# Optimization experiments

Measured on AMD Instinct MI355X. Metric: run time of the kernel, lower is better.

Reference implementation:

```python
import jax, jax.numpy as jnp
import numpy as np

N = 50000      # query points
N0 = 50000     # support points
M = 32         # neighbors per query
K = 15         # kernel points
DIM = 3
D_IN = 64
D_OUT = 64
POINT_INFLUENCE = 1.0
KERNEL_RADIUS = 1.5 * POINT_INFLUENCE  # _INFLUENCE_TO_RADIUS * point_influence


def setup_inputs() -> dict:
    key = jax.random.key(0)
    k1, k2, k3, k4, k5 = jax.random.split(key, 5)
    query_points = jax.random.normal(k1, (N, DIM), jnp.float32)
    support_points = jax.random.normal(k2, (N0, DIM), jnp.float32)
    neighbors = jax.random.randint(k3, (N, M), 0, N0 + 1)  # index N0 = shadow point
    x = jax.random.normal(k4, (N0, D_IN), jnp.float32)
    # Kernel point dispositions: fixed center point, rest spread within kernel radius
    # (stand-in for kernel_point_optimization_debug; K_points is a frozen parameter).
    rng = np.random.RandomState(0)
    kp = rng.uniform(-1.0, 1.0, (K, DIM))
    kp[0, :] = 0.0
    kp = kp * (KERNEL_RADIUS / np.max(np.linalg.norm(kp, axis=1)))
    K_points = jnp.asarray(kp, dtype=jnp.float32)
    # Xavier-normal conv weights [K, D_IN, D_OUT]
    std = (2.0 / (D_IN + D_OUT)) ** 0.5
    weight = jax.random.normal(k5, (K, D_IN, D_OUT), jnp.float32) * std
    return {
        "query_points": query_points,
        "support_points": support_points,
        "neighbors": neighbors,
        "x": x,
        "K_points": K_points,
        "weight": weight,
    }


def reference(query_points, support_points, neighbors, x, K_points, weight):
    # Shadow support point far away + zero shadow feature row
    shadow = jnp.full((1, query_points.shape[1]), 1e6, dtype=support_points.dtype)
    sp = jnp.concatenate([support_points, shadow], axis=0)            # [N0+1, 3]
    xp = jnp.concatenate([x, jnp.zeros((1, x.shape[1]), x.dtype)], axis=0)  # [N0+1, d]

    # Gather neighbor coords, center on query point
    neighb_pts = sp[neighbors] - query_points[:, None, :]             # [N, M, 3]
    # Squared distances to each kernel point
    diff = neighb_pts[:, :, None, :] - K_points[None, None, :, :]     # [N, M, K, 3]
    sq_distances = jnp.sum(diff * diff, axis=-1)                      # [N, M, K]

    # Linear influence, then transpose to [N, K, M]
    all_weights = jnp.clip(1.0 - jnp.sqrt(sq_distances) / POINT_INFLUENCE, 0.0)
    all_weights = jnp.swapaxes(all_weights, 1, 2)                     # [N, K, M]

    # Gather neighbor features and aggregate per kernel point
    feats = xp[neighbors]                                             # [N, M, d]
    weighted = jnp.einsum("nkm,nmd->nkd", all_weights, feats)        # [N, K, d]
    # Apply per-kernel-point weight matrices and sum over kernel points
    out = jnp.einsum("nkd,kdo->no", weighted, weight)                # [N, out]
    return out
```

## Files before the change

### kernel.cpp

```cpp
#include <hip/hip_runtime.h>

#define NQ 50000
#define NS 50000
#define MNB 32
#define KP 15
#define DF 64
#define WTS 968

typedef __bf16 bf16x8 __attribute__((ext_vector_type(8)));
typedef float  f32x4  __attribute__((ext_vector_type(4)));

__device__ __forceinline__ unsigned short f2bf(float f) {
    union { float f; unsigned int u; } v; v.f = f;
    unsigned int u = v.u;
    return (unsigned short)((u + 0x7FFFu + ((u >> 16) & 1u)) >> 16);
}

__global__ __launch_bounds__(256) void conv_w(const float* __restrict__ W,
                                              uint4* __restrict__ wBf) {
    const int chunk = blockIdx.x * 256 + threadIdx.x;
    if (chunk >= 7680) return;
    const int t = chunk >> 6, c = chunk & 63;
    union { unsigned short s[8]; uint4 u; } pk;
    #pragma unroll
    for (int j = 0; j < 8; ++j)
        pk.s[j] = f2bf(W[(size_t)(t * 8 + j) * 64 + c]);
    wBf[chunk] = pk.u;
}

__global__ __launch_bounds__(1024, 8) void kpconv_fused(
    const float* __restrict__ qp, const float* __restrict__ sp,
    const int* __restrict__ nb, const float* __restrict__ x,
    const float* __restrict__ kpts, const uint4* __restrict__ wBf,
    float* __restrict__ out)
{
    __shared__ struct {
        __align__(16) unsigned short wt[16 * WTS];
        __align__(16) float w[16][33][20];
        __align__(16) unsigned int am[16][MNB];
    } sm;

    const int tid  = threadIdx.x;
    const int lane = tid & 63, wv = tid >> 6;
    const int kh = lane >> 5, m = lane & 31;
    const int n0 = blockIdx.x * 16;
    const int n  = n0 + wv;

    if (lane < 20) sm.w[wv][32][lane] = 0.0f;

    const int id = nb[n * MNB + m];
    const float qx = qp[n * 3 + 0], qy = qp[n * 3 + 1], qz = qp[n * 3 + 2];
    float sx = 1e6f, sy = 1e6f, sz = 1e6f;
    if (id < NS) { sx = sp[id * 3 + 0]; sy = sp[id * 3 + 1]; sz = sp[id * 3 + 2]; }
    const float rx = sx - qx, ry = sy - qy, rz = sz - qz;
    float wk[8], wmax = 0.0f;
    const int kbase = kh * 8;
    #pragma unroll
    for (int j = 0; j < 8; ++j) {
        const int k = kbase + j;
        const int kc = (k < KP) ? k : 0;
        const float dx = rx - kpts[kc * 3 + 0];
        const float dy = ry - kpts[kc * 3 + 1];
        const float dz = rz - kpts[kc * 3 + 2];
        float wkj = fmaxf(1.0f - sqrtf(dx * dx + dy * dy + dz * dz), 0.0f);
        if (k >= KP) wkj = 0.0f;
        wk[j] = wkj;
        wmax = fmaxf(wmax, wkj);
    }
    const unsigned long long bal = __ballot(wmax > 0.0f);
    const unsigned int comb = (unsigned int)(bal & 0xFFFFFFFFull) |
                              (unsigned int)(bal >> 32);
    const int A = __popc(comb);
    const int Apad = (A + 3) & ~3;
    const bool act = (comb >> m) & 1u;
    if (act) {
        float4* wr = (float4*)&sm.w[wv][m][0];
        wr[kh * 2 + 0] = make_float4(wk[0], wk[1], wk[2], wk[3]);
        wr[kh * 2 + 1] = make_float4(wk[4], wk[5], wk[6], wk[7]);
    }
    if (kh == 0) {
        if (act) {
            const int pos = __popc(comb & ((1u << m) - 1u));
            sm.am[wv][pos] = ((unsigned)id << 6) | (unsigned)m;
        }
        if (m < Apad - A) sm.am[wv][A + m] = 32u;
    }

    const int d = lane;
    float acc[KP];
    #pragma unroll
    for (int k = 0; k < KP; ++k) acc[k] = 0.0f;

#define ACC1(EE, FF)                                                        \
    {                                                                       \
        const float4* wr = (const float4*)&sm.w[wv][(EE) & 63u][0];         \
        const float4 w0 = wr[0], w1 = wr[1], w2 = wr[2], w3 = wr[3];        \
        acc[0]  += (FF) * w0.x;  acc[1]  += (FF) * w0.y;                    \
        acc[2]  += (FF) * w0.z;  acc[3]  += (FF) * w0.w;                    \
        acc[4]  += (FF) * w1.x;  acc[5]  += (FF) * w1.y;                    \
        acc[6]  += (FF) * w1.z;  acc[7]  += (FF) * w1.w;                    \
        acc[8]  += (FF) * w2.x;  acc[9]  += (FF) * w2.y;                    \
        acc[10] += (FF) * w2.z;  acc[11] += (FF) * w2.w;                    \
        acc[12] += (FF) * w3.x;  acc[13] += (FF) * w3.y;  acc[14] += (FF) * w3.z; \
    }

    for (int j0 = 0; j0 < Apad; j0 += 4) {
        const uint4 e = *(const uint4*)&sm.am[wv][j0];
        const float f0 = x[(size_t)(e.x >> 6) * DF + d];
        const float f1 = x[(size_t)(e.y >> 6) * DF + d];
        const float f2 = x[(size_t)(e.z >> 6) * DF + d];
        const float f3 = x[(size_t)(e.w >> 6) * DF + d];
        ACC1(e.x, f0) ACC1(e.y, f1) ACC1(e.z, f2) ACC1(e.w, f3)
    }
#undef ACC1

    unsigned short* wrow = sm.wt + wv * WTS + d;
    #pragma unroll
    for (int k = 0; k < KP; ++k)
        wrow[k * DF] = f2bf(acc[k]);

    __syncthreads();
    if (wv >= 4) return;

    const int cl = lane & 15, q = lane >> 4;
    f32x4 dacc = (f32x4){0.f, 0.f, 0.f, 0.f};
    #pragma unroll 6
    for (int ks = 0; ks < 30; ++ks) {
        const bf16x8 a = *(const bf16x8*)&sm.wt[cl * WTS + ks * 32 + q * 8];
        union { uint4 u; bf16x8 v; } bu;
        bu.u = wBf[(4 * ks + q) * 64 + wv * 16 + cl];
        dacc = __builtin_amdgcn_mfma_f32_16x16x32_bf16(a, bu.v, dacc, 0, 0, 0);
    }
    #pragma unroll
    for (int i = 0; i < 4; ++i)
        out[(size_t)(n0 + q * 4 + i) * 64 + wv * 16 + cl] = dacc[i];
}

extern "C" void kernel_launch(void* const* d_in, const int* in_sizes, int n_in,
                              void* d_out, int out_size, void* d_ws, size_t ws_size,
                              hipStream_t stream) {
    const float* qp   = (const float*)d_in[0];
    const float* sp   = (const float*)d_in[1];
    const int*   nb   = (const int*)d_in[2];
    const float* x    = (const float*)d_in[3];
    const float* kpts = (const float*)d_in[4];
    const float* W    = (const float*)d_in[5];
    float* out = (float*)d_out;

    uint4* wBf = (uint4*)d_ws;

    hipLaunchKernelGGL(conv_w, dim3(30), dim3(256), 0, stream, W, wBf);
    hipLaunchKernelGGL(kpconv_fused, dim3(NQ / 16), dim3(1024), 0, stream,
                       qp, sp, nb, x, kpts, wBf, out);
}
```

Measured before the change: 140.6 us.

## Aggregate neighbor features with bf16 MFMA over pre-converted bf16 features

Replaces the per-lane scalar FMA loop that accumulated neighbor features into 15 kernel-point sums with a single 16x16x32 bf16 MFMA per 16-channel block. Neighbor weights are stored as bf16 in shared memory and neighbor features are gathered from a bf16 copy of x made by a new conversion kernel each call. The conv weight layout is permuted to match the new intermediate ordering. The ballot-based compaction that skipped inactive neighbors is dropped, so all 32 neighbors are always gathered. It also adds a full read and write pass over x and rounds features to bf16, which lowers precision.

```diff
diff --git a/kernel.cpp b/kernel.cpp
--- a/kernel.cpp
+++ b/kernel.cpp
@@ -6,6 +6,7 @@
 #define KP 15
 #define DF 64
 #define WTS 968
+#define WQS 40
 
 typedef __bf16 bf16x8 __attribute__((ext_vector_type(8)));
 typedef float  f32x4  __attribute__((ext_vector_type(4)));
@@ -16,28 +17,48 @@
     return (unsigned short)((u + 0x7FFFu + ((u >> 16) & 1u)) >> 16);
 }
 
+__global__ __launch_bounds__(256) void conv_x(const float* __restrict__ x,
+                                              unsigned int* __restrict__ xb, int n4) {
+    const int i = blockIdx.x * 256 + threadIdx.x;
+    if (i * 4 + 3 < n4) {
+        const float4* s = (const float4*)x + i * 2;
+        const float4 a0 = s[0], a1 = s[1];
+        uint4 o;
+        o.x = (unsigned)f2bf(a0.x) | ((unsigned)f2bf(a0.y) << 16);
+        o.y = (unsigned)f2bf(a0.z) | ((unsigned)f2bf(a0.w) << 16);
+        o.z = (unsigned)f2bf(a1.x) | ((unsigned)f2bf(a1.y) << 16);
+        o.w = (unsigned)f2bf(a1.z) | ((unsigned)f2bf(a1.w) << 16);
+        ((uint4*)xb)[i] = o;
+    }
+}
+
 __global__ __launch_bounds__(256) void conv_w(const float* __restrict__ W,
                                               uint4* __restrict__ wBf) {
     const int chunk = blockIdx.x * 256 + threadIdx.x;
     if (chunk >= 7680) return;
-    const int t = chunk >> 6, c = chunk & 63;
+    const int tc = chunk >> 6, c = chunk & 63;
     union { unsigned short s[8]; uint4 u; } pk;
     #pragma unroll
-    for (int j = 0; j < 8; ++j)
-        pk.s[j] = f2bf(W[(size_t)(t * 8 + j) * 64 + c]);
+    for (int j = 0; j < 8; ++j) {
+        const int kappa = tc * 8 + j;
+        const int k  = kappa >> 6;
+        const int cb = kappa & 3;
+        const int t  = (kappa >> 2) & 15;
+        pk.s[j] = f2bf(W[(size_t)(k * 64 + cb * 16 + t) * 64 + c]);
+    }
     wBf[chunk] = pk.u;
 }
 
 __global__ __launch_bounds__(1024, 8) void kpconv_fused(
     const float* __restrict__ qp, const float* __restrict__ sp,
-    const int* __restrict__ nb, const float* __restrict__ x,
+    const int* __restrict__ nb, const unsigned short* __restrict__ xbu,
     const float* __restrict__ kpts, const uint4* __restrict__ wBf,
     float* __restrict__ out)
 {
     __shared__ struct {
         __align__(16) unsigned short wt[16 * WTS];
-        __align__(16) float w[16][33][20];
-        __align__(16) unsigned int am[16][MNB];
+        __align__(16) unsigned short wq[16][16 * WQS];
+        __align__(16) unsigned int   ids[16][MNB];
     } sm;
 
     const int tid  = threadIdx.x;
@@ -46,83 +67,66 @@
     const int n0 = blockIdx.x * 16;
     const int n  = n0 + wv;
 
-    if (lane < 20) sm.w[wv][32][lane] = 0.0f;
-
     const int id = nb[n * MNB + m];
     const float qx = qp[n * 3 + 0], qy = qp[n * 3 + 1], qz = qp[n * 3 + 2];
     float sx = 1e6f, sy = 1e6f, sz = 1e6f;
     if (id < NS) { sx = sp[id * 3 + 0]; sy = sp[id * 3 + 1]; sz = sp[id * 3 + 2]; }
     const float rx = sx - qx, ry = sy - qy, rz = sz - qz;
-    float wk[8], wmax = 0.0f;
-    const int kbase = kh * 8;
+    float wk[8];
     #pragma unroll
     for (int j = 0; j < 8; ++j) {
-        const int k = kbase + j;
+        const int k = kh * 8 + j;
         const int kc = (k < KP) ? k : 0;
         const float dx = rx - kpts[kc * 3 + 0];
         const float dy = ry - kpts[kc * 3 + 1];
         const float dz = rz - kpts[kc * 3 + 2];
-        float wkj = fmaxf(1.0f - sqrtf(dx * dx + dy * dy + dz * dz), 0.0f);
-        if (k >= KP) wkj = 0.0f;
-        wk[j] = wkj;
-        wmax = fmaxf(wmax, wkj);
+        wk[j] = fmaxf(1.0f - sqrtf(dx * dx + dy * dy + dz * dz), 0.0f);
     }
-    const unsigned long long bal = __ballot(wmax > 0.0f);
-    const unsigned int comb = (unsigned int)(bal & 0xFFFFFFFFull) |
-                              (unsigned int)(bal >> 32);
-    const int A = __popc(comb);
-    const int Apad = (A + 3) & ~3;
-    const bool act = (comb >> m) & 1u;
-    if (act) {
-        float4* wr = (float4*)&sm.w[wv][m][0];
-        wr[kh * 2 + 0] = make_float4(wk[0], wk[1], wk[2], wk[3]);
-        wr[kh * 2 + 1] = make_float4(wk[4], wk[5], wk[6], wk[7]);
+    #pragma unroll
+    for (int j = 0; j < 8; ++j) {
+        const int k = kh * 8 + j;
+        if (k < KP) sm.wq[wv][k * WQS + m] = f2bf(wk[j]);
     }
-    if (kh == 0) {
-        if (act) {
-            const int pos = __popc(comb & ((1u << m) - 1u));
-            sm.am[wv][pos] = ((unsigned)id << 6) | (unsigned)m;
-        }
-        if (m < Apad - A) sm.am[wv][A + m] = 32u;
+    if (kh == 0) sm.ids[wv][m] = (id < NS) ? (unsigned)id : 0u;
+
+    const int cl = lane & 15, q = lane >> 4;
+    union { uint4 u; bf16x8 v; } af;
+    af.u = *(const uint4*)&sm.wq[wv][cl * WQS + q * 8];
+    const uint4 ia = *(const uint4*)&sm.ids[wv][q * 8];
+    const uint4 ib = *(const uint4*)&sm.ids[wv][q * 8 + 4];
+    const f32x4 zero = (f32x4){0.f, 0.f, 0.f, 0.f};
+    f32x4 acc1[4];
+    #pragma unroll
+    for (int cb = 0; cb < 4; ++cb) {
+        const unsigned v0 = xbu[(size_t)ia.x * DF + cb * 16 + cl];
+        const unsigned v1 = xbu[(size_t)ia.y * DF + cb * 16 + cl];
+        const unsigned v2 = xbu[(size_t)ia.z * DF + cb * 16 + cl];
+        const unsigned v3 = xbu[(size_t)ia.w * DF + cb * 16 + cl];
+        const unsigned v4 = xbu[(size_t)ib.x * DF + cb * 16 + cl];
+        const unsigned v5 = xbu[(size_t)ib.y * DF + cb * 16 + cl];
+        const unsigned v6 = xbu[(size_t)ib.z * DF + cb * 16 + cl];
+        const unsigned v7 = xbu[(size_t)ib.w * DF + cb * 16 + cl];
+        union { uint4 u; bf16x8 v; } bf;
+        bf.u.x = v0 | (v1 << 16);
+        bf.u.y = v2 | (v3 << 16);
+        bf.u.z = v4 | (v5 << 16);
+        bf.u.w = v6 | (v7 << 16);
+        acc1[cb] = __builtin_amdgcn_mfma_f32_16x16x32_bf16(af.v, bf.v, zero, 0, 0, 0);
     }
 
-    const int d = lane;
-    float acc[KP];
     #pragma unroll
-    for (int k = 0; k < KP; ++k) acc[k] = 0.0f;
-
-#define ACC1(EE, FF)                                                        \
-    {                                                                       \
-        const float4* wr = (const float4*)&sm.w[wv][(EE) & 63u][0];         \
-        const float4 w0 = wr[0], w1 = wr[1], w2 = wr[2], w3 = wr[3];        \
-        acc[0]  += (FF) * w0.x;  acc[1]  += (FF) * w0.y;                    \
-        acc[2]  += (FF) * w0.z;  acc[3]  += (FF) * w0.w;                    \
-        acc[4]  += (FF) * w1.x;  acc[5]  += (FF) * w1.y;                    \
-        acc[6]  += (FF) * w1.z;  acc[7]  += (FF) * w1.w;                    \
-        acc[8]  += (FF) * w2.x;  acc[9]  += (FF) * w2.y;                    \
-        acc[10] += (FF) * w2.z;  acc[11] += (FF) * w2.w;                    \
-        acc[12] += (FF) * w3.x;  acc[13] += (FF) * w3.y;  acc[14] += (FF) * w3.z; \
+    for (int i = 0; i < 4; ++i) {
+        const int k = q * 4 + i;
+        if (k < KP) {
+            union { unsigned short s[4]; uint2 u; } pk;
+            #pragma unroll
+            for (int cb = 0; cb < 4; ++cb) pk.s[cb] = f2bf(acc1[cb][i]);
+            *(uint2*)&sm.wt[wv * WTS + (k * 16 + cl) * 4] = pk.u;
+        }
     }
-
-    for (int j0 = 0; j0 < Apad; j0 += 4) {
-        const uint4 e = *(const uint4*)&sm.am[wv][j0];
-        const float f0 = x[(size_t)(e.x >> 6) * DF + d];
-        const float f1 = x[(size_t)(e.y >> 6) * DF + d];
-        const float f2 = x[(size_t)(e.z >> 6) * DF + d];
-        const float f3 = x[(size_t)(e.w >> 6) * DF + d];
-        ACC1(e.x, f0) ACC1(e.y, f1) ACC1(e.z, f2) ACC1(e.w, f3)
-    }
-#undef ACC1
-
-    unsigned short* wrow = sm.wt + wv * WTS + d;
-    #pragma unroll
-    for (int k = 0; k < KP; ++k)
-        wrow[k * DF] = f2bf(acc[k]);
-
     __syncthreads();
     if (wv >= 4) return;
 
-    const int cl = lane & 15, q = lane >> 4;
     f32x4 dacc = (f32x4){0.f, 0.f, 0.f, 0.f};
     #pragma unroll 6
     for (int ks = 0; ks < 30; ++ks) {
@@ -147,9 +151,12 @@
     const float* W    = (const float*)d_in[5];
     float* out = (float*)d_out;
 
-    uint4* wBf = (uint4*)d_ws;
+    uint4*          wBf = (uint4*)d_ws;
+    unsigned int*   xb  = (unsigned int*)((char*)d_ws + 122880);
+    unsigned short* xbu = (unsigned short*)xb;
 
+    hipLaunchKernelGGL(conv_x, dim3(1563), dim3(256), 0, stream, x, xb, NS * DF / 2);
     hipLaunchKernelGGL(conv_w, dim3(30), dim3(256), 0, stream, W, wBf);
     hipLaunchKernelGGL(kpconv_fused, dim3(NQ / 16), dim3(1024), 0, stream,
-                       qp, sp, nb, x, kpts, wBf, out);
+                       qp, sp, nb, xbu, kpts, wBf, out);
 }
```

After: 136.2 us. 1.03x faster.
